# Optimization experiments

Measured on AMD Instinct MI355X. Metric: run time of the kernel, lower is better.

The kernel has to match this reference:

```python
import jax
import jax.numpy as jnp
import numpy as np
from jax import lax

TOKENS = 65536
D = 512
E = 8
H = 2048


def setup_inputs() -> dict:
    key = jax.random.key(0)
    ks = jax.random.split(key, 6)
    inp = {
        "x": jax.random.normal(ks[0], (TOKENS, D), dtype=jnp.float32),
        "router_w": jax.random.normal(ks[1], (D, E), dtype=jnp.float32) * 0.02,
        "router_b": jnp.zeros((E,), dtype=jnp.float32),
        "w1": jax.random.normal(ks[2], (E, D, H), dtype=jnp.float32) * 0.02,
        "b1": jnp.zeros((E, H), dtype=jnp.float32),
        "w2": jax.random.normal(ks[3], (E, H, D), dtype=jnp.float32) * 0.02,
        "b2": jnp.zeros((E, D), dtype=jnp.float32),
        "act_expert_num": 2,
    }
    return inp


def reference(x, router_w, router_b, w1, b1, w2, b2, act_expert_num):
    B = x.shape[0]
    # Router: Linear + Softmax over experts
    probs = jax.nn.softmax(x @ router_w + router_b, axis=-1)  # [B, E]
    rw, sel = lax.top_k(probs, act_expert_num)                # [B, k]
    rw = rw / jnp.sum(rw, axis=-1, keepdims=True)             # renormalize top-k
    # Dense combine weights per expert: comb[b, e] = sum_k rw[b,k] * [sel[b,k]==e]
    comb = jnp.zeros((B, E), dtype=x.dtype).at[
        jnp.arange(B)[:, None], sel
    ].add(rw)                                                 # [B, E]

    def body(acc, params):
        w1e, b1e, w2e, b2e, ce = params
        h = jax.nn.relu(x @ w1e + b1e)        # [B, H]
        y = h @ w2e + b2e                     # [B, D]
        return acc + ce[:, None] * y, None

    out, _ = lax.scan(body, jnp.zeros_like(x), (w1, b1, w2, b2, comb.T))
    return out
```

## Files before the change

### kernel.cpp

```cpp
#include <hip/hip_runtime.h>
#include <hip/hip_bf16.h>

constexpr int B = 65536;
constexpr int D = 512;
constexpr int E = 8;
constexpr int H = 2048;
constexpr int CT_ST = 140;

typedef __bf16 bf16x8 __attribute__((ext_vector_type(8)));
typedef float  f32x4  __attribute__((ext_vector_type(4)));

__device__ __forceinline__ unsigned short f2bf(float f) {
    unsigned u = __float_as_uint(f);
    u += 0x7FFFu + ((u >> 16) & 1u);
    return (unsigned short)(u >> 16);
}

__device__ __forceinline__ void dma16(const void* g, void* lds) {
    auto* gp = reinterpret_cast<const __attribute__((address_space(1))) unsigned*>(
        reinterpret_cast<uintptr_t>(g));
    auto* lp = reinterpret_cast<__attribute__((address_space(3))) unsigned*>(
        reinterpret_cast<uintptr_t>(lds));
    __builtin_amdgcn_global_load_lds(gp, lp, 16, 0, 0);
}

__global__ __launch_bounds__(256) void convert_x(
    const float* __restrict__ x, unsigned short* __restrict__ xb) {
    const size_t i = ((size_t)blockIdx.x * 256 + threadIdx.x) * 8;
    const float4 v0 = *(const float4*)(x + i);
    const float4 v1 = *(const float4*)(x + i + 4);
    uint4 p;
    p.x = (unsigned)f2bf(v0.x) | ((unsigned)f2bf(v0.y) << 16);
    p.y = (unsigned)f2bf(v0.z) | ((unsigned)f2bf(v0.w) << 16);
    p.z = (unsigned)f2bf(v1.x) | ((unsigned)f2bf(v1.y) << 16);
    p.w = (unsigned)f2bf(v1.z) | ((unsigned)f2bf(v1.w) << 16);
    *(uint4*)(xb + i) = p;
}

__global__ __launch_bounds__(128) void router2(
    const float* __restrict__ x, const float* __restrict__ rw,
    const float* __restrict__ rb, unsigned* __restrict__ cnt,
    unsigned* __restrict__ tok_list, float* __restrict__ w_list) {
    __shared__ unsigned lcnt[E];
    __shared__ unsigned gbase[E];
    const int tid = threadIdx.x;
    if (tid < E) lcnt[tid] = 0u;
    __syncthreads();

    const int t = blockIdx.x * 128 + tid;
    const float4* xr = (const float4*)(x + (size_t)t * D);
    float acc[E];
#pragma unroll
    for (int e = 0; e < E; ++e) acc[e] = 0.f;

    for (int i = 0; i < D / 4; ++i) {
        const float4 xv = xr[i];
        const float* wr = rw + (size_t)i * 4 * E;
#pragma unroll
        for (int e = 0; e < E; ++e) {
            acc[e] += xv.x * wr[e] + xv.y * wr[E + e] + xv.z * wr[2 * E + e]
                    + xv.w * wr[3 * E + e];
        }
    }
#pragma unroll
    for (int e = 0; e < E; ++e) acc[e] += rb[e];

    int e0 = 0; float l0 = acc[0];
#pragma unroll
    for (int e = 1; e < E; ++e) if (acc[e] > l0) { l0 = acc[e]; e0 = e; }
    int e1 = -1; float l1 = -3.4e38f;
#pragma unroll
    for (int e = 0; e < E; ++e)
        if (e != e0 && acc[e] > l1) { l1 = acc[e]; e1 = e; }

    const float w0 = 1.f / (1.f + expf(l1 - l0));
    const float w1v = 1.f - w0;

    const unsigned r0 = atomicAdd(&lcnt[e0], 1u);
    const unsigned r1 = atomicAdd(&lcnt[e1], 1u);
    __syncthreads();
    if (tid < E) gbase[tid] = atomicAdd(&cnt[tid], lcnt[tid]);
    __syncthreads();
    const unsigned s0 = gbase[e0] + r0;
    const unsigned s1 = gbase[e1] + r1;
    tok_list[(size_t)e0 * B + s0] = (unsigned)t;  w_list[(size_t)e0 * B + s0] = w0;
    tok_list[(size_t)e1 * B + s1] = (unsigned)t;  w_list[(size_t)e1 * B + s1] = w1v;
}

__global__ __launch_bounds__(128) void pad_counts(
    const unsigned* __restrict__ cnt, unsigned* __restrict__ cntp,
    unsigned* __restrict__ tok_list, float* __restrict__ w_list, int cap) {
    const int tid = threadIdx.x;
    for (int e = 0; e < E; ++e) {
        const unsigned c = cnt[e];
        unsigned p = (c + 127u) & ~127u;
        if (p > (unsigned)cap) p = (unsigned)cap;
        if (c + tid < p) {
            tok_list[(size_t)e * B + c + tid] = 0u;
            w_list[(size_t)e * B + c + tid] = 0.f;
        }
        if (tid == 0) cntp[e] = p;
    }
}

__global__ __launch_bounds__(256) void transpose_bf16(
    const float* __restrict__ in, unsigned short* __restrict__ outp,
    int R, int C) {
    __shared__ unsigned short T[64][72];
    const int e = blockIdx.z;
    const int c0 = blockIdx.x * 64, r0 = blockIdx.y * 64;
    const float* ine = in + (size_t)e * R * C;
    unsigned short* oute = outp + (size_t)e * R * C;
    const int tid = threadIdx.x;
    const int rl = tid >> 2, cl = (tid & 3) * 16;

    const float* src = ine + (size_t)(r0 + rl) * C + c0 + cl;
    unsigned pk[8];
#pragma unroll
    for (int i = 0; i < 4; ++i) {
        const float4 v = *(const float4*)(src + i * 4);
        pk[2 * i]     = (unsigned)f2bf(v.x) | ((unsigned)f2bf(v.y) << 16);
        pk[2 * i + 1] = (unsigned)f2bf(v.z) | ((unsigned)f2bf(v.w) << 16);
    }
    *(uint4*)(&T[rl][cl])     = make_uint4(pk[0], pk[1], pk[2], pk[3]);
    *(uint4*)(&T[rl][cl + 8]) = make_uint4(pk[4], pk[5], pk[6], pk[7]);
    __syncthreads();

    unsigned po[8];
#pragma unroll
    for (int j = 0; j < 8; ++j) {
        po[j] = (unsigned)T[cl + 2 * j][rl] | ((unsigned)T[cl + 2 * j + 1][rl] << 16);
    }
    unsigned short* dst = oute + (size_t)(c0 + rl) * R + r0 + cl;
    *(uint4*)(dst)     = make_uint4(po[0], po[1], po[2], po[3]);
    *(uint4*)(dst + 8) = make_uint4(po[4], po[5], po[6], po[7]);
}

struct alignas(16) StageBufs {
    unsigned short A[2][128 * 32];
    unsigned short Bm[2][128 * 32];
};
union SmemU {
    StageBufs st;
    unsigned short Ct[64 * CT_ST];
};

__global__ __launch_bounds__(256, 4) void stage_kernel(
    const unsigned short* __restrict__ xb,
    const unsigned short* __restrict__ w1s, const unsigned short* __restrict__ w2s,
    const float* __restrict__ b1, const float* __restrict__ b2,
    const unsigned* __restrict__ cntp,
    const unsigned* __restrict__ tok_list, const float* __restrict__ w_list,
    unsigned short* __restrict__ hb_w, const unsigned short* __restrict__ hb_r,
    float* __restrict__ out, int e_w, int e_r) {
    __shared__ SmemU sm;
    __shared__ int   s_toks[128];
    __shared__ float s_wgts[128];
    const int tid = threadIdx.x, wv = tid >> 6, lane = tid & 63;
    const int ln = lane & 15, q = lane >> 4;
    const int wm = wv & 1, wn = wv >> 1;
    const int r4 = lane >> 2, pc = lane & 3;
    const int m0 = blockIdx.x * 128;
    const int dst0 = (wv * 2 + 0) * 512;
    const int dst1 = (wv * 2 + 1) * 512;
    const int qs  = q  ^ ((ln >> 1) & 3);
    const int pcs = pc ^ ((r4 >> 1) & 3);

    f32x4 acc[4][4];
#pragma unroll
    for (int i = 0; i < 4; ++i)
#pragma unroll
        for (int j = 0; j < 4; ++j) acc[i][j] = (f32x4){0.f, 0.f, 0.f, 0.f};

    if (blockIdx.y >= 4) {
        if (e_w < 0) return;
        const int e = e_w;
        if ((unsigned)m0 >= cntp[e]) return;
        const int n0 = (blockIdx.y - 4) * 128;
        const size_t base = (size_t)e * B;
        constexpr int NT = D / 32;

        const unsigned ta0 = tok_list[base + m0 + (wv * 2 + 0) * 16 + r4];
        const unsigned ta1 = tok_list[base + m0 + (wv * 2 + 1) * 16 + r4];
        const unsigned short* ap0 = xb + (size_t)ta0 * D + pcs * 8;
        const unsigned short* ap1 = xb + (size_t)ta1 * D + pcs * 8;
        const unsigned short* w1e = w1s + (size_t)e * H * D;
        const unsigned short* bp0 = w1e + (size_t)(n0 + (wv * 2 + 0) * 16 + r4) * D + pcs * 8;
        const unsigned short* bp1 = w1e + (size_t)(n0 + (wv * 2 + 1) * 16 + r4) * D + pcs * 8;

        unsigned short *A0 = sm.st.A[0], *A1 = sm.st.A[1];
        unsigned short *B0 = sm.st.Bm[0], *B1 = sm.st.Bm[1];

        dma16(ap0, A0 + dst0);  dma16(ap1, A0 + dst1);
        dma16(bp0, B0 + dst0);  dma16(bp1, B0 + dst1);

        for (int t = 0; t < NT; ++t) {
            asm volatile("s_waitcnt vmcnt(0)" ::: "memory");
            __builtin_amdgcn_s_barrier();
            asm volatile("" ::: "memory");
            if (t + 1 < NT) {
                const int nk = (t + 1) * 32;
                dma16(ap0 + nk, A1 + dst0);  dma16(ap1 + nk, A1 + dst1);
                dma16(bp0 + nk, B1 + dst0);  dma16(bp1 + nk, B1 + dst1);
            }
            bf16x8 af[4], bfr[4];
#pragma unroll
            for (int i = 0; i < 4; ++i) {
                af[i]  = *(const bf16x8*)(A0 + (wm * 64 + i * 16 + ln) * 32 + qs * 8);
                bfr[i] = *(const bf16x8*)(B0 + (wn * 64 + i * 16 + ln) * 32 + qs * 8);
            }
            __builtin_amdgcn_s_setprio(1);
#pragma unroll
            for (int mt = 0; mt < 4; ++mt)
#pragma unroll
                for (int nt = 0; nt < 4; ++nt)
                    acc[mt][nt] = __builtin_amdgcn_mfma_f32_16x16x32_bf16(
                        af[mt], bfr[nt], acc[mt][nt], 0, 0, 0);
            __builtin_amdgcn_s_setprio(0);
            unsigned short* tp;
            tp = A0; A0 = A1; A1 = tp;
            tp = B0; B0 = B1; B1 = tp;
        }
        __syncthreads();

        float b1v[4];
#pragma unroll
        for (int nt = 0; nt < 4; ++nt)
            b1v[nt] = b1[(size_t)e * H + n0 + wn * 64 + nt * 16 + ln];

#pragma unroll
        for (int c = 0; c < 2; ++c) {
            if (wm == c) {
#pragma unroll
                for (int mt = 0; mt < 4; ++mt)
#pragma unroll
                    for (int nt = 0; nt < 4; ++nt)
#pragma unroll
                        for (int r = 0; r < 4; ++r) {
                            const int lr = mt * 16 + q * 4 + r;
                            float v = acc[mt][nt][r] + b1v[nt];
                            v = v > 0.f ? v : 0.f;
                            sm.Ct[lr * CT_ST + wn * 64 + nt * 16 + ln] = f2bf(v);
                        }
            }
            __syncthreads();
            {
                const int lr = tid >> 2, seg = tid & 3;
                const unsigned short* csrc = sm.Ct + lr * CT_ST + seg * 32;
                unsigned short* gdst = hb_w + (size_t)(m0 + c * 64 + lr) * H + n0 + seg * 32;
#pragma unroll
                for (int u = 0; u < 4; ++u)
                    *(uint4*)(gdst + u * 8) = *(const uint4*)(csrc + u * 8);
            }
            __syncthreads();
        }
    } else {
        if (e_r < 0) return;
        const int e = e_r;
        if ((unsigned)m0 >= cntp[e]) return;
        const int n0 = blockIdx.y * 128;
        const size_t base = (size_t)e * B;
        constexpr int NT = H / 32;

        if (tid < 128) {
            s_toks[tid] = (int)tok_list[base + m0 + tid];
            s_wgts[tid] = w_list[base + m0 + tid];
        }
        const unsigned short* ap0 = hb_r + (size_t)(m0 + (wv * 2 + 0) * 16 + r4) * H + pcs * 8;
        const unsigned short* ap1 = hb_r + (size_t)(m0 + (wv * 2 + 1) * 16 + r4) * H + pcs * 8;
        const unsigned short* w2e = w2s + (size_t)e * D * H;
        const unsigned short* bp0 = w2e + (size_t)(n0 + (wv * 2 + 0) * 16 + r4) * H + pcs * 8;
        const unsigned short* bp1 = w2e + (size_t)(n0 + (wv * 2 + 1) * 16 + r4) * H + pcs * 8;

        unsigned short *A0 = sm.st.A[0], *A1 = sm.st.A[1];
        unsigned short *B0 = sm.st.Bm[0], *B1 = sm.st.Bm[1];

        dma16(ap0, A0 + dst0);  dma16(ap1, A0 + dst1);
        dma16(bp0, B0 + dst0);  dma16(bp1, B0 + dst1);

        for (int t = 0; t < NT; ++t) {
            asm volatile("s_waitcnt vmcnt(0)" ::: "memory");
            __builtin_amdgcn_s_barrier();
            asm volatile("" ::: "memory");
            if (t + 1 < NT) {
                const int nk = (t + 1) * 32;
                dma16(ap0 + nk, A1 + dst0);  dma16(ap1 + nk, A1 + dst1);
                dma16(bp0 + nk, B1 + dst0);  dma16(bp1 + nk, B1 + dst1);
            }
            bf16x8 af[4], bfr[4];
#pragma unroll
            for (int i = 0; i < 4; ++i) {
                af[i]  = *(const bf16x8*)(A0 + (wm * 64 + i * 16 + ln) * 32 + qs * 8);
                bfr[i] = *(const bf16x8*)(B0 + (wn * 64 + i * 16 + ln) * 32 + qs * 8);
            }
            __builtin_amdgcn_s_setprio(1);
#pragma unroll
            for (int mt = 0; mt < 4; ++mt)
#pragma unroll
                for (int nt = 0; nt < 4; ++nt)
                    acc[mt][nt] = __builtin_amdgcn_mfma_f32_16x16x32_bf16(
                        af[mt], bfr[nt], acc[mt][nt], 0, 0, 0);
            __builtin_amdgcn_s_setprio(0);
            unsigned short* tp;
            tp = A0; A0 = A1; A1 = tp;
            tp = B0; B0 = B1; B1 = tp;
        }
        __syncthreads();

        float b2v[4];
#pragma unroll
        for (int nt = 0; nt < 4; ++nt)
            b2v[nt] = b2[(size_t)e * D + n0 + wn * 64 + nt * 16 + ln];

#pragma unroll
        for (int mt = 0; mt < 4; ++mt) {
#pragma unroll
            for (int r = 0; r < 4; ++r) {
                const int m = wm * 64 + mt * 16 + q * 4 + r;
                const float wgt = s_wgts[m];
                if (wgt != 0.f) {
                    const int tok = s_toks[m];
                    float* orow = out + (size_t)tok * D + n0 + wn * 64 + ln;
#pragma unroll
                    for (int nt = 0; nt < 4; ++nt)
                        orow[nt * 16] += wgt * (acc[mt][nt][r] + b2v[nt]);
                }
            }
        }
    }
}

extern "C" void kernel_launch(void* const* d_in, const int* in_sizes, int n_in,
                              void* d_out, int out_size, void* d_ws, size_t ws_size,
                              hipStream_t stream) {
    const float* x  = (const float*)d_in[0];
    const float* rw = (const float*)d_in[1];
    const float* rb = (const float*)d_in[2];
    const float* w1 = (const float*)d_in[3];
    const float* b1 = (const float*)d_in[4];
    const float* w2 = (const float*)d_in[5];
    const float* b2 = (const float*)d_in[6];
    float* out = (float*)d_out;

    char* ws = (char*)d_ws;
    const size_t off_tok = 1024;
    const size_t off_wl  = off_tok + (size_t)E * B * 4;
    const size_t off_w1s = off_wl  + (size_t)E * B * 4;
    const size_t off_w2s = off_w1s + (size_t)E * D * H * 2;
    const size_t off_xb  = off_w2s + (size_t)E * D * H * 2;
    const size_t off_hb  = off_xb  + (size_t)B * D * 2;

    unsigned* cnt      = (unsigned*)ws;
    unsigned* cntp     = (unsigned*)(ws + 256);
    unsigned* tok_list = (unsigned*)(ws + off_tok);
    float*    w_list   = (float*)(ws + off_wl);
    unsigned short* w1s = (unsigned short*)(ws + off_w1s);
    unsigned short* w2s = (unsigned short*)(ws + off_w2s);
    unsigned short* xb  = (unsigned short*)(ws + off_xb);

    const size_t rem = (ws_size > off_hb) ? (ws_size - off_hb) : 0;
    const size_t hrow = (size_t)H * 2;
    int cap; bool pipelined;
    {
        size_t cp = (rem / 2 / hrow) & ~(size_t)127;
        if (cp > 24576) cp = 24576;
        if (cp >= 20480) { pipelined = true; cap = (int)cp; }
        else {
            pipelined = false;
            size_t cs = (rem / hrow) & ~(size_t)127;
            if (cs > 24576) cs = 24576;
            cap = (int)cs;
        }
    }
    unsigned short* hb0 = (unsigned short*)(ws + off_hb);
    unsigned short* hb1 = pipelined ? hb0 + (size_t)cap * H : hb0;

    hipMemsetAsync(ws, 0, 1024, stream);
    hipMemsetAsync(d_out, 0, (size_t)out_size * sizeof(float), stream);

    convert_x<<<(B * D) / 2048, 256, 0, stream>>>(x, xb);
    transpose_bf16<<<dim3(H / 64, D / 64, E), 256, 0, stream>>>(w1, w1s, D, H);
    transpose_bf16<<<dim3(D / 64, H / 64, E), 256, 0, stream>>>(w2, w2s, H, D);
    router2<<<B / 128, 128, 0, stream>>>(x, rw, rb, cnt, tok_list, w_list);
    pad_counts<<<1, 128, 0, stream>>>(cnt, cntp, tok_list, w_list, cap);

    const dim3 sgrid(cap / 128, 20);
    if (pipelined) {
        for (int s = 0; s <= E; ++s) {
            unsigned short* hw = (s & 1) ? hb1 : hb0;
            unsigned short* hr = (s & 1) ? hb0 : hb1;
            stage_kernel<<<sgrid, 256, 0, stream>>>(
                xb, w1s, w2s, b1, b2, cntp, tok_list, w_list,
                hw, hr, out, (s < E) ? s : -1, (s > 0) ? s - 1 : -1);
        }
    } else {
        for (int e = 0; e < E; ++e) {
            stage_kernel<<<sgrid, 256, 0, stream>>>(
                xb, w1s, w2s, b1, b2, cntp, tok_list, w_list,
                hb0, hb0, out, e, -1);
            stage_kernel<<<sgrid, 256, 0, stream>>>(
                xb, w1s, w2s, b1, b2, cntp, tok_list, w_list,
                hb0, hb0, out, -1, e);
        }
    }
}
```

Baseline: 1.255 ms.

## Store weights and hidden activations in K-blocked 32-wide panels for contiguous DMA

Weights are packed into K-panels of 32 elements (panel-major, then row), and the hidden buffer is written in the same panel layout. Each K-step's tile loads then come from one contiguous 128x32 region instead of strided rows with large pitch. This is meant to improve DRAM/L2 locality and cut TLB pressure on the global_load_lds DMA. The cost is a more scattered epilogue store pattern for the hidden buffer, plus a cap parameter threaded through every launch.

```diff
diff --git a/kernel.cpp b/kernel.cpp
--- a/kernel.cpp
+++ b/kernel.cpp
@@ -103,7 +103,7 @@
     }
 }
 
-__global__ __launch_bounds__(256) void transpose_bf16(
+__global__ __launch_bounds__(256) void pack_bf16(
     const float* __restrict__ in, unsigned short* __restrict__ outp,
     int R, int C) {
     __shared__ unsigned short T[64][72];
@@ -131,7 +131,8 @@
     for (int j = 0; j < 8; ++j) {
         po[j] = (unsigned)T[cl + 2 * j][rl] | ((unsigned)T[cl + 2 * j + 1][rl] << 16);
     }
-    unsigned short* dst = oute + (size_t)(c0 + rl) * R + r0 + cl;
+    unsigned short* dst = oute + ((size_t)((r0 + cl) >> 5) * C + (c0 + rl)) * 32
+                               + ((r0 + cl) & 31);
     *(uint4*)(dst)     = make_uint4(po[0], po[1], po[2], po[3]);
     *(uint4*)(dst + 8) = make_uint4(po[4], po[5], po[6], po[7]);
 }
@@ -147,12 +148,12 @@
 
 __global__ __launch_bounds__(256, 4) void stage_kernel(
     const unsigned short* __restrict__ xb,
-    const unsigned short* __restrict__ w1s, const unsigned short* __restrict__ w2s,
+    const unsigned short* __restrict__ w1p, const unsigned short* __restrict__ w2p,
     const float* __restrict__ b1, const float* __restrict__ b2,
     const unsigned* __restrict__ cntp,
     const unsigned* __restrict__ tok_list, const float* __restrict__ w_list,
     unsigned short* __restrict__ hb_w, const unsigned short* __restrict__ hb_r,
-    float* __restrict__ out, int e_w, int e_r) {
+    float* __restrict__ out, int e_w, int e_r, int cap) {
     __shared__ SmemU sm;
     __shared__ int   s_toks[128];
     __shared__ float s_wgts[128];
@@ -184,9 +185,10 @@
         const unsigned ta1 = tok_list[base + m0 + (wv * 2 + 1) * 16 + r4];
         const unsigned short* ap0 = xb + (size_t)ta0 * D + pcs * 8;
         const unsigned short* ap1 = xb + (size_t)ta1 * D + pcs * 8;
-        const unsigned short* w1e = w1s + (size_t)e * H * D;
-        const unsigned short* bp0 = w1e + (size_t)(n0 + (wv * 2 + 0) * 16 + r4) * D + pcs * 8;
-        const unsigned short* bp1 = w1e + (size_t)(n0 + (wv * 2 + 1) * 16 + r4) * D + pcs * 8;
+        const unsigned short* w1e = w1p + (size_t)e * H * D;
+        const unsigned short* bp0 = w1e + (size_t)(n0 + (wv * 2 + 0) * 16 + r4) * 32 + pcs * 8;
+        const unsigned short* bp1 = w1e + (size_t)(n0 + (wv * 2 + 1) * 16 + r4) * 32 + pcs * 8;
+        const size_t bstep = (size_t)H * 32;
 
         unsigned short *A0 = sm.st.A[0], *A1 = sm.st.A[1];
         unsigned short *B0 = sm.st.Bm[0], *B1 = sm.st.Bm[1];
@@ -199,9 +201,10 @@
             __builtin_amdgcn_s_barrier();
             asm volatile("" ::: "memory");
             if (t + 1 < NT) {
-                const int nk = (t + 1) * 32;
-                dma16(ap0 + nk, A1 + dst0);  dma16(ap1 + nk, A1 + dst1);
-                dma16(bp0 + nk, B1 + dst0);  dma16(bp1 + nk, B1 + dst1);
+                const int ka = (t + 1) * 32;
+                const size_t kb = (size_t)(t + 1) * bstep;
+                dma16(ap0 + ka, A1 + dst0);  dma16(ap1 + ka, A1 + dst1);
+                dma16(bp0 + kb, B1 + dst0);  dma16(bp1 + kb, B1 + dst1);
             }
             bf16x8 af[4], bfr[4];
 #pragma unroll
@@ -245,12 +248,16 @@
             }
             __syncthreads();
             {
-                const int lr = tid >> 2, seg = tid & 3;
-                const unsigned short* csrc = sm.Ct + lr * CT_ST + seg * 32;
-                unsigned short* gdst = hb_w + (size_t)(m0 + c * 64 + lr) * H + n0 + seg * 32;
-#pragma unroll
-                for (int u = 0; u < 4; ++u)
-                    *(uint4*)(gdst + u * 8) = *(const uint4*)(csrc + u * 8);
+                const int cc = wv;
+#pragma unroll
+                for (int u = 0; u < 4; ++u) {
+                    const int sr = u * 16 + (lane >> 2);
+                    const unsigned short* csrc = sm.Ct + sr * CT_ST + cc * 32 + (lane & 3) * 8;
+                    unsigned short* gdst = hb_w
+                        + ((size_t)((n0 >> 5) + cc) * cap + (m0 + c * 64 + sr)) * 32
+                        + (lane & 3) * 8;
+                    *(uint4*)gdst = *(const uint4*)csrc;
+                }
             }
             __syncthreads();
         }
@@ -266,11 +273,13 @@
             s_toks[tid] = (int)tok_list[base + m0 + tid];
             s_wgts[tid] = w_list[base + m0 + tid];
         }
-        const unsigned short* ap0 = hb_r + (size_t)(m0 + (wv * 2 + 0) * 16 + r4) * H + pcs * 8;
-        const unsigned short* ap1 = hb_r + (size_t)(m0 + (wv * 2 + 1) * 16 + r4) * H + pcs * 8;
-        const unsigned short* w2e = w2s + (size_t)e * D * H;
-        const unsigned short* bp0 = w2e + (size_t)(n0 + (wv * 2 + 0) * 16 + r4) * H + pcs * 8;
-        const unsigned short* bp1 = w2e + (size_t)(n0 + (wv * 2 + 1) * 16 + r4) * H + pcs * 8;
+        const unsigned short* ap0 = hb_r + (size_t)(m0 + (wv * 2 + 0) * 16 + r4) * 32 + pcs * 8;
+        const unsigned short* ap1 = hb_r + (size_t)(m0 + (wv * 2 + 1) * 16 + r4) * 32 + pcs * 8;
+        const unsigned short* w2e = w2p + (size_t)e * D * H;
+        const unsigned short* bp0 = w2e + (size_t)(n0 + (wv * 2 + 0) * 16 + r4) * 32 + pcs * 8;
+        const unsigned short* bp1 = w2e + (size_t)(n0 + (wv * 2 + 1) * 16 + r4) * 32 + pcs * 8;
+        const size_t astep = (size_t)cap * 32;
+        const size_t bstep = (size_t)D * 32;
 
         unsigned short *A0 = sm.st.A[0], *A1 = sm.st.A[1];
         unsigned short *B0 = sm.st.Bm[0], *B1 = sm.st.Bm[1];
@@ -283,9 +292,10 @@
             __builtin_amdgcn_s_barrier();
             asm volatile("" ::: "memory");
             if (t + 1 < NT) {
-                const int nk = (t + 1) * 32;
-                dma16(ap0 + nk, A1 + dst0);  dma16(ap1 + nk, A1 + dst1);
-                dma16(bp0 + nk, B1 + dst0);  dma16(bp1 + nk, B1 + dst1);
+                const size_t ka = (size_t)(t + 1) * astep;
+                const size_t kb = (size_t)(t + 1) * bstep;
+                dma16(ap0 + ka, A1 + dst0);  dma16(ap1 + ka, A1 + dst1);
+                dma16(bp0 + kb, B1 + dst0);  dma16(bp1 + kb, B1 + dst1);
             }
             bf16x8 af[4], bfr[4];
 #pragma unroll
@@ -379,8 +389,8 @@
     hipMemsetAsync(d_out, 0, (size_t)out_size * sizeof(float), stream);
 
     convert_x<<<(B * D) / 2048, 256, 0, stream>>>(x, xb);
-    transpose_bf16<<<dim3(H / 64, D / 64, E), 256, 0, stream>>>(w1, w1s, D, H);
-    transpose_bf16<<<dim3(D / 64, H / 64, E), 256, 0, stream>>>(w2, w2s, H, D);
+    pack_bf16<<<dim3(H / 64, D / 64, E), 256, 0, stream>>>(w1, w1s, D, H);
+    pack_bf16<<<dim3(D / 64, H / 64, E), 256, 0, stream>>>(w2, w2s, H, D);
     router2<<<B / 128, 128, 0, stream>>>(x, rw, rb, cnt, tok_list, w_list);
     pad_counts<<<1, 128, 0, stream>>>(cnt, cntp, tok_list, w_list, cap);
 
@@ -391,16 +401,16 @@
             unsigned short* hr = (s & 1) ? hb0 : hb1;
             stage_kernel<<<sgrid, 256, 0, stream>>>(
                 xb, w1s, w2s, b1, b2, cntp, tok_list, w_list,
-                hw, hr, out, (s < E) ? s : -1, (s > 0) ? s - 1 : -1);
+                hw, hr, out, (s < E) ? s : -1, (s > 0) ? s - 1 : -1, cap);
         }
     } else {
         for (int e = 0; e < E; ++e) {
             stage_kernel<<<sgrid, 256, 0, stream>>>(
                 xb, w1s, w2s, b1, b2, cntp, tok_list, w_list,
-                hb0, hb0, out, e, -1);
+                hb0, hb0, out, e, -1, cap);
             stage_kernel<<<sgrid, 256, 0, stream>>>(
                 xb, w1s, w2s, b1, b2, cntp, tok_list, w_list,
-                hb0, hb0, out, -1, e);
-        }
-    }
-}
+                hb0, hb0, out, -1, e, cap);
+        }
+    }
+}
```

Result: faster. 1.151 ms (-8.3%).
